# Kernel tuning notes

Measured on AMD Instinct MI355X. Metric: run time of the kernel, lower is better.

## Reference

```python
import jax, jax.numpy as jnp
import numpy as np

B, N, M = 2, 2048, 2048
Q_DIM = 1024
HEADS = 8
DIM_HEAD = 64
INNER = HEADS * DIM_HEAD  # 512


def setup_inputs() -> dict:
    key = jax.random.key(0)
    ks = jax.random.split(key, 7)
    s_in = 1.0 / np.sqrt(Q_DIM)
    s_out = 1.0 / np.sqrt(INNER)
    return {
        "x": jax.random.normal(ks[0], (B, N, Q_DIM), dtype=jnp.float32),
        "context": jax.random.normal(ks[1], (B, M, Q_DIM), dtype=jnp.float32),
        "Wq": jax.random.normal(ks[2], (Q_DIM, INNER), dtype=jnp.float32) * s_in,
        "Wk": jax.random.normal(ks[3], (Q_DIM, INNER), dtype=jnp.float32) * s_in,
        "Wv": jax.random.normal(ks[4], (Q_DIM, INNER), dtype=jnp.float32) * s_in,
        "Wo": jax.random.normal(ks[5], (INNER, Q_DIM), dtype=jnp.float32) * s_out,
        "bo": jax.random.normal(ks[6], (Q_DIM,), dtype=jnp.float32) * 0.01,
    }


def reference(x, context, Wq, Wk, Wv, Wo, bo):
    scale = DIM_HEAD ** (-0.5)
    # projections, split heads: [b, n, inner] -> [b, h, n, d]
    def split_heads(t):
        b, n, _ = t.shape
        return t.reshape(b, n, HEADS, DIM_HEAD).transpose(0, 2, 1, 3)
    q = split_heads(x @ Wq)
    k = split_heads(context @ Wk)
    v = split_heads(context @ Wv)
    sim = jnp.einsum('bhid,bhjd->bhij', q, k) * scale  # [b,h,n,m] full score matrix
    attn = jax.nn.softmax(sim, axis=-1)
    out = jnp.einsum('bhij,bhjd->bhid', attn, v)       # [b,h,n,d]
    out = out.transpose(0, 2, 1, 3).reshape(x.shape[0], x.shape[1], INNER)
    return out @ Wo + bo
```

## Files before the change

kernel.cpp:

```cpp
#include <hip/hip_runtime.h>

typedef __attribute__((ext_vector_type(8))) short short8;
typedef __attribute__((ext_vector_type(4))) short bf16x4;
typedef __attribute__((ext_vector_type(4))) float floatx4;
typedef __attribute__((ext_vector_type(4))) float f32x4;

__device__ __forceinline__ short f2bf(float f) {
    union { float f; unsigned u; } v;
    v.f = f;
    unsigned r = v.u + 0x7fffu + ((v.u >> 16) & 1u);
    return (short)(r >> 16);
}
__device__ __forceinline__ short8 cvt8(f32x4 a, f32x4 b) {
    short8 r;
    r[0] = f2bf(a[0]); r[1] = f2bf(a[1]); r[2] = f2bf(a[2]); r[3] = f2bf(a[3]);
    r[4] = f2bf(b[0]); r[5] = f2bf(b[1]); r[6] = f2bf(b[2]); r[7] = f2bf(b[3]);
    return r;
}
__device__ __forceinline__ bf16x4 pack4(float a, float b, float c, float d) {
    union { float f; unsigned u; } x;
    unsigned ua, ub, uc, ud;
    x.f = a; ua = (x.u + 0x8000u) >> 16;
    x.f = b; ub = (x.u + 0x8000u) >> 16;
    x.f = c; uc = (x.u + 0x8000u) >> 16;
    x.f = d; ud = (x.u + 0x8000u) >> 16;
    union { bf16x4 s; unsigned u2[2]; } r;
    r.u2[0] = ua | (ub << 16);
    r.u2[1] = uc | (ud << 16);
    return r.s;
}

#define MFMA_BF16(a, b, c) __builtin_amdgcn_mfma_f32_16x16x32_bf16((a), (b), (c), 0, 0, 0)

__device__ __forceinline__ floatx4 mfma16(bf16x4 a, bf16x4 b, floatx4 c) {
#if __has_builtin(__builtin_amdgcn_mfma_f32_16x16x16bf16_1k)
    return __builtin_amdgcn_mfma_f32_16x16x16bf16_1k(a, b, c, 0, 0, 0);
#else
    floatx4 d;
    asm volatile("v_mfma_f32_16x16x16_bf16 %0, %1, %2, %3"
                 : "=&v"(d) : "v"(a), "v"(b), "v"(c));
    return d;
#endif
}

__device__ __forceinline__ float fast_exp2(float x) {
#if __has_builtin(__builtin_amdgcn_exp2f)
    return __builtin_amdgcn_exp2f(x);
#else
    return exp2f(x);
#endif
}

#define QSCALE_LOG2E 0.18033688011112042f

__global__ __launch_bounds__(256) void wfrag_all(const float* __restrict__ Wq,
                                                 const float* __restrict__ Wk,
                                                 const float* __restrict__ Wv,
                                                 const float* __restrict__ Wo,
                                                 short* __restrict__ WqF,
                                                 short* __restrict__ WkF,
                                                 short* __restrict__ WvF,
                                                 short* __restrict__ WoF) {
    const int z = blockIdx.y;
    const float* src = (z == 0) ? Wq : (z == 1) ? Wk : (z == 2) ? Wv : Wo;
    short* dst = (z == 0) ? WqF : (z == 1) ? WkF : (z == 2) ? WvF : WoF;
    const int nbits = (z < 3) ? 9 : 10;
    const int N = 1 << nbits;
    const int t = blockIdx.x * 256 + threadIdx.x;
    const int kb = t >> nbits;
    const int n = t & (N - 1);
    const float* s = src + (size_t)(kb * 8) * N + n;
    short8 v;
#pragma unroll
    for (int j = 0; j < 8; ++j) v[j] = f2bf(s[(size_t)j * N]);
    *(short8*)(dst + (size_t)t * 8) = v;
}

__global__ __launch_bounds__(256, 3) void gemm_qkv(const float* __restrict__ x,
                                                   const float* __restrict__ ctx,
                                                   const short* __restrict__ WqF,
                                                   const short* __restrict__ WkF,
                                                   const short* __restrict__ WvF,
                                                   short* __restrict__ Qw,
                                                   short* __restrict__ Kw,
                                                   short* __restrict__ Vtw) {
    const int z = blockIdx.z;
    const float* A  = (z == 0) ? x : ctx;
    const short* WF = (z == 0) ? WqF : (z == 1) ? WkF : WvF;
    const int tid = threadIdx.x;
    const int w = tid >> 6;
    const int lane = tid & 63;
    const int quad = lane >> 4, ln = lane & 15;
    const int wr = w >> 1, wc = w & 1;
    const int row0 = blockIdx.x * 64;
    const int col0 = blockIdx.y * 128;

    __shared__ __align__(16) short Alds[2][2048];

    const int srow = tid >> 2;
    const int sseg = tid & 3;
    const float* aG = A + (size_t)(row0 + srow) * 1024 + sseg * 8;

    const short* bG[4];
#pragma unroll
    for (int t = 0; t < 4; ++t)
        bG[t] = WF + ((size_t)quad * 512 + col0 + wc * 64 + t * 16 + ln) * 8;

    floatx4 acc[2][4] = {};
    f32x4 aR[2][2];
    short8 bR[2][4];

    auto loadA = [&](int it, int set) {
        aR[set][0] = *(const f32x4*)(aG + it * 32);
        aR[set][1] = *(const f32x4*)(aG + it * 32 + 4);
    };
    auto writeA = [&](int buf, int set) {
        *(short8*)(&Alds[buf][(sseg * 64 + srow) * 8]) = cvt8(aR[set][0], aR[set][1]);
    };
    auto loadB = [&](int it, int set) {
#pragma unroll
        for (int t = 0; t < 4; ++t)
            bR[set][t] = *(const short8*)(bG[t] + (size_t)it * 16384);
    };

    loadA(0, 0);
    writeA(0, 0);
    loadA(1, 1);
    loadB(0, 0);
    __syncthreads();

    const int nsteps = 1024 / 32;
    for (int it = 0; it < nsteps; ++it) {
        const int buf = it & 1;
        if (it + 2 < nsteps) loadA(it + 2, it & 1);
        if (it + 1 < nsteps) {
            loadB(it + 1, (it + 1) & 1);
            writeA(buf ^ 1, (it + 1) & 1);
        }
        short8 af[2];
#pragma unroll
        for (int i = 0; i < 2; ++i)
            af[i] = *(const short8*)(&Alds[buf][quad * 512 + (wr * 32 + i * 16 + ln) * 8]);
#pragma unroll
        for (int i = 0; i < 2; ++i)
#pragma unroll
            for (int t = 0; t < 4; ++t)
                acc[i][t] = MFMA_BF16(af[i], bR[it & 1][t], acc[i][t]);
        __syncthreads();
    }

    const float oscale = (z == 0) ? QSCALE_LOG2E : 1.0f;
    short* dst = (z == 0) ? Qw : (z == 1) ? Kw : Vtw;
#pragma unroll
    for (int i = 0; i < 2; ++i)
#pragma unroll
        for (int t = 0; t < 4; ++t)
#pragma unroll
            for (int r = 0; r < 4; ++r) {
                const int R = row0 + wr * 32 + i * 16 + quad * 4 + r;
                const int C = col0 + wc * 64 + t * 16 + ln;
                const int b = R >> 11, n = R & 2047;
                const int h = C >> 6, d = C & 63;
                const short val = f2bf(acc[i][t][r] * oscale);
                if (z < 2)
                    dst[((b * 8 + h) * 2048 + n) * 64 + d] = val;
                else
                    dst[((b * 8 + h) * 64 + d) * 2048 + n] = val;
            }
}

__global__ __launch_bounds__(256, 2) void attn_kernel(const short* __restrict__ Q,
                                                      const short* __restrict__ K,
                                                      const short* __restrict__ Vt,
                                                      short* __restrict__ Aw) {
    const int tid = threadIdx.x;
    const int w = tid >> 6;
    const int lane = tid & 63;
    const int quad = lane >> 4;
    const int ln = lane & 15;
    const int q0 = blockIdx.x * 64;
    const int bh = blockIdx.y;

    __shared__ __align__(16) short klds[2][64][72];
    __shared__ __align__(16) short vlds[2][64][72];

    const short* Qbh = Q + bh * 2048 * 64;
    const short* Kbh = K + bh * 2048 * 64;
    const short* Vbh = Vt + bh * 64 * 2048;

    short8 qf[2];
    {
        const int qrow = q0 + w * 16 + ln;
        qf[0] = *(const short8*)(Qbh + qrow * 64 + quad * 8);
        qf[1] = *(const short8*)(Qbh + qrow * 64 + 32 + quad * 8);
    }

    floatx4 ot[4] = {};
    float lp = 0.f;

    const int sr = tid >> 3;
    const int sc = (tid & 7) * 8;

    auto computeTile = [&](int b) {
        short8 kf[8];
#pragma unroll
        for (int t = 0; t < 4; ++t)
#pragma unroll
            for (int ks = 0; ks < 2; ++ks)
                kf[t * 2 + ks] = *(const short8*)(&klds[b][t * 16 + ln][ks * 32 + quad * 8]);
        bf16x4 vf[16];
#pragma unroll
        for (int dt = 0; dt < 4; ++dt)
#pragma unroll
            for (int t = 0; t < 4; ++t)
                vf[dt * 4 + t] = *(const bf16x4*)(&vlds[b][dt * 16 + ln][t * 16 + quad * 4]);

        floatx4 s[4] = {};
#pragma unroll
        for (int ks = 0; ks < 2; ++ks)
#pragma unroll
            for (int t = 0; t < 4; ++t)
                s[t] = MFMA_BF16(kf[t * 2 + ks], qf[ks], s[t]);

        bf16x4 pf[4];
#pragma unroll
        for (int t = 0; t < 4; ++t) {
            float p0 = fast_exp2(s[t][0]);
            float p1 = fast_exp2(s[t][1]);
            float p2 = fast_exp2(s[t][2]);
            float p3 = fast_exp2(s[t][3]);
            lp += (p0 + p1) + (p2 + p3);
            pf[t] = pack4(p0, p1, p2, p3);
        }
#pragma unroll
        for (int t = 0; t < 4; ++t)
#pragma unroll
            for (int dt = 0; dt < 4; ++dt)
                ot[dt] = mfma16(vf[dt * 4 + t], pf[t], ot[dt]);
    };

    const int nt = 2048 / 64;

    {
        short8 k0 = *(const short8*)(Kbh + tid * 8);
        short8 k1 = *(const short8*)(Kbh + (tid + 256) * 8);
        short8 v0 = *(const short8*)(Vbh + sr * 2048 + sc);
        short8 v1 = *(const short8*)(Vbh + (sr + 32) * 2048 + sc);
        *(short8*)(&klds[0][sr][sc]) = k0;
        *(short8*)(&klds[0][sr + 32][sc]) = k1;
        *(short8*)(&vlds[0][sr][sc]) = v0;
        *(short8*)(&vlds[0][sr + 32][sc]) = v1;
    }
    __syncthreads();

    for (int it = 0; it < nt; ++it) {
        short8 k0, k1, v0, v1;
        const bool more = (it + 1 < nt);
        if (more) {
            const int jn = (it + 1) * 64;
            k0 = *(const short8*)(Kbh + jn * 64 + tid * 8);
            k1 = *(const short8*)(Kbh + jn * 64 + (tid + 256) * 8);
            v0 = *(const short8*)(Vbh + sr * 2048 + jn + sc);
            v1 = *(const short8*)(Vbh + (sr + 32) * 2048 + jn + sc);
        }
        computeTile(it & 1);
        if (more) {
            const int nb = (it + 1) & 1;
            *(short8*)(&klds[nb][sr][sc]) = k0;
            *(short8*)(&klds[nb][sr + 32][sc]) = k1;
            *(short8*)(&vlds[nb][sr][sc]) = v0;
            *(short8*)(&vlds[nb][sr + 32][sc]) = v1;
        }
        __syncthreads();
    }

    lp += __shfl_xor(lp, 16);
    lp += __shfl_xor(lp, 32);
    const float invL = 1.0f / lp;

    const int n = q0 + w * 16 + ln;
    const int b = bh >> 3, h = bh & 7;
    short* abase = Aw + ((size_t)(b * 2048 + n) * 512) + h * 64 + quad * 4;
#pragma unroll
    for (int dt = 0; dt < 4; ++dt)
        *(bf16x4*)(abase + dt * 16) =
            pack4(ot[dt][0] * invL, ot[dt][1] * invL, ot[dt][2] * invL, ot[dt][3] * invL);
}

__global__ __launch_bounds__(256, 2) void gemm_final(const short* __restrict__ A,
                                                     const short* __restrict__ WoF,
                                                     const float* __restrict__ bias,
                                                     float* __restrict__ out) {
    const int tid = threadIdx.x;
    const int w = tid >> 6;
    const int lane = tid & 63;
    const int quad = lane >> 4, ln = lane & 15;
    const int wr = w >> 1, wc = w & 1;
    const int row0 = blockIdx.x * 64;
    const int col0 = blockIdx.y * 128;

    __shared__ __align__(16) short Alds[2][2048];

    const int srow = tid >> 2;
    const int sseg = tid & 3;
    const short* aG = A + (size_t)(row0 + srow) * 512 + sseg * 8;

    const short* bG[4];
#pragma unroll
    for (int t = 0; t < 4; ++t)
        bG[t] = WoF + ((size_t)quad * 1024 + col0 + wc * 64 + t * 16 + ln) * 8;

    floatx4 acc[2][4] = {};
    short8 aR[2];
    short8 bR[2][4];

    auto loadA = [&](int it, int set) { aR[set] = *(const short8*)(aG + it * 32); };
    auto writeA = [&](int buf, int set) {
        *(short8*)(&Alds[buf][(sseg * 64 + srow) * 8]) = aR[set];
    };
    auto loadB = [&](int it, int set) {
#pragma unroll
        for (int t = 0; t < 4; ++t)
            bR[set][t] = *(const short8*)(bG[t] + (size_t)it * 32768);
    };

    loadA(0, 0);
    writeA(0, 0);
    loadA(1, 1);
    loadB(0, 0);
    __syncthreads();

    const int nsteps = 512 / 32;
    for (int it = 0; it < nsteps; ++it) {
        const int buf = it & 1;
        if (it + 2 < nsteps) loadA(it + 2, it & 1);
        if (it + 1 < nsteps) {
            loadB(it + 1, (it + 1) & 1);
            writeA(buf ^ 1, (it + 1) & 1);
        }
        short8 af[2];
#pragma unroll
        for (int i = 0; i < 2; ++i)
            af[i] = *(const short8*)(&Alds[buf][quad * 512 + (wr * 32 + i * 16 + ln) * 8]);
#pragma unroll
        for (int i = 0; i < 2; ++i)
#pragma unroll
            for (int t = 0; t < 4; ++t)
                acc[i][t] = MFMA_BF16(af[i], bR[it & 1][t], acc[i][t]);
        __syncthreads();
    }

#pragma unroll
    for (int i = 0; i < 2; ++i)
#pragma unroll
        for (int t = 0; t < 4; ++t)
#pragma unroll
            for (int r = 0; r < 4; ++r) {
                const int R = row0 + wr * 32 + i * 16 + quad * 4 + r;
                const int C = col0 + wc * 64 + t * 16 + ln;
                out[(size_t)R * 1024 + C] = acc[i][t][r] + bias[C];
            }
}

extern "C" void kernel_launch(void* const* d_in, const int* in_sizes, int n_in,
                              void* d_out, int out_size, void* d_ws, size_t ws_size,
                              hipStream_t stream) {
    const float* x   = (const float*)d_in[0];
    const float* ctx = (const float*)d_in[1];
    const float* Wq  = (const float*)d_in[2];
    const float* Wk  = (const float*)d_in[3];
    const float* Wv  = (const float*)d_in[4];
    const float* Wo  = (const float*)d_in[5];
    const float* bo  = (const float*)d_in[6];
    float* out = (float*)d_out;

    char* ws = (char*)d_ws;
    size_t off = 0;
    auto alloc = [&](size_t bytes) { char* p = ws + off; off += (bytes + 255) & ~(size_t)255; return p; };

    short* WqF  = (short*)alloc(512 * 1024 * 2);
    short* WkF  = (short*)alloc(512 * 1024 * 2);
    short* WvF  = (short*)alloc(512 * 1024 * 2);
    short* WoF  = (short*)alloc(1024 * 512 * 2);
    short* Qw   = (short*)alloc((size_t)16 * 2048 * 64 * 2);
    short* Kw   = (short*)alloc((size_t)16 * 2048 * 64 * 2);
    short* Vtw  = (short*)alloc((size_t)16 * 2048 * 64 * 2);
    short* Aw   = (short*)alloc((size_t)4096 * 512 * 2);

    wfrag_all<<<dim3(256, 4), 256, 0, stream>>>(Wq, Wk, Wv, Wo, WqF, WkF, WvF, WoF);

    gemm_qkv<<<dim3(64, 4, 3), 256, 0, stream>>>(x, ctx, WqF, WkF, WvF, Qw, Kw, Vtw);

    attn_kernel<<<dim3(32, 16), 256, 0, stream>>>(Qw, Kw, Vtw, Aw);

    gemm_final<<<dim3(64, 8), 256, 0, stream>>>(Aw, WoF, bo, out);
}
```

Baseline: 167.9 us.

## Pre-convert activations to fragment-major bf16 layout and drop LDS staging in GEMMs

```diff
diff --git a/kernel.cpp b/kernel.cpp
--- a/kernel.cpp
+++ b/kernel.cpp
@@ -76,8 +76,42 @@
     *(short8*)(dst + (size_t)t * 8) = v;
 }
 
-__global__ __launch_bounds__(256, 3) void gemm_qkv(const float* __restrict__ x,
-                                                   const float* __restrict__ ctx,
+__global__ __launch_bounds__(256) void afrag(const float* __restrict__ x,
+                                             const float* __restrict__ ctx,
+                                             short* __restrict__ AxF,
+                                             short* __restrict__ AcF) {
+    const float* src = (blockIdx.z == 0) ? x : ctx;
+    short* dst = (blockIdx.z == 0) ? AxF : AcF;
+    const int r0 = blockIdx.x * 64;
+    const int k0 = blockIdx.y * 64;
+    __shared__ short tile[64][72];
+    const int tid = threadIdx.x;
+    {
+        const int seg = tid & 15;
+        const int rbase = tid >> 4;
+#pragma unroll
+        for (int i = 0; i < 4; ++i) {
+            const int row = rbase + i * 16;
+            f32x4 v = *(const f32x4*)(src + (size_t)(r0 + row) * 1024 + k0 + seg * 4);
+#pragma unroll
+            for (int jj = 0; jj < 4; ++jj) tile[row][seg * 4 + jj] = f2bf(v[jj]);
+        }
+    }
+    __syncthreads();
+    {
+        const int kbl = tid >> 5;
+        const int rbase = tid & 31;
+#pragma unroll
+        for (int j = 0; j < 2; ++j) {
+            const int row = rbase + j * 32;
+            short8 v = *(const short8*)(&tile[row][kbl * 8]);
+            *(short8*)(dst + ((size_t)(k0 / 8 + kbl) * 4096 + r0 + row) * 8) = v;
+        }
+    }
+}
+
+__global__ __launch_bounds__(256, 4) void gemm_qkv(const short* __restrict__ AxF,
+                                                   const short* __restrict__ AcF,
                                                    const short* __restrict__ WqF,
                                                    const short* __restrict__ WkF,
                                                    const short* __restrict__ WvF,
@@ -85,7 +119,7 @@
                                                    short* __restrict__ Kw,
                                                    short* __restrict__ Vtw) {
     const int z = blockIdx.z;
-    const float* A  = (z == 0) ? x : ctx;
+    const short* AF = (z == 0) ? AxF : AcF;
     const short* WF = (z == 0) ? WqF : (z == 1) ? WkF : WvF;
     const int tid = threadIdx.x;
     const int w = tid >> 6;
@@ -95,58 +129,33 @@
     const int row0 = blockIdx.x * 64;
     const int col0 = blockIdx.y * 128;
 
-    __shared__ __align__(16) short Alds[2][2048];
-
-    const int srow = tid >> 2;
-    const int sseg = tid & 3;
-    const float* aG = A + (size_t)(row0 + srow) * 1024 + sseg * 8;
-
-    const short* bG[4];
-#pragma unroll
-    for (int t = 0; t < 4; ++t)
-        bG[t] = WF + ((size_t)quad * 512 + col0 + wc * 64 + t * 16 + ln) * 8;
+    const short* aBase = AF + ((size_t)quad * 4096 + row0 + wr * 32 + ln) * 8;
+    const short* bBase = WF + ((size_t)quad * 512 + col0 + wc * 64 + ln) * 8;
 
     floatx4 acc[2][4] = {};
-    f32x4 aR[2][2];
-    short8 bR[2][4];
-
-    auto loadA = [&](int it, int set) {
-        aR[set][0] = *(const f32x4*)(aG + it * 32);
-        aR[set][1] = *(const f32x4*)(aG + it * 32 + 4);
+    short8 aR[3][2], bR[3][4];
+
+    auto loadStep = [&](int it) {
+        const int s = it % 3;
+#pragma unroll
+        for (int i = 0; i < 2; ++i)
+            aR[s][i] = *(const short8*)(aBase + (size_t)it * 131072 + i * 128);
+#pragma unroll
+        for (int t = 0; t < 4; ++t)
+            bR[s][t] = *(const short8*)(bBase + (size_t)it * 16384 + t * 128);
     };
-    auto writeA = [&](int buf, int set) {
-        *(short8*)(&Alds[buf][(sseg * 64 + srow) * 8]) = cvt8(aR[set][0], aR[set][1]);
-    };
-    auto loadB = [&](int it, int set) {
-#pragma unroll
-        for (int t = 0; t < 4; ++t)
-            bR[set][t] = *(const short8*)(bG[t] + (size_t)it * 16384);
-    };
-
-    loadA(0, 0);
-    writeA(0, 0);
-    loadA(1, 1);
-    loadB(0, 0);
-    __syncthreads();
-
-    const int nsteps = 1024 / 32;
-    for (int it = 0; it < nsteps; ++it) {
-        const int buf = it & 1;
-        if (it + 2 < nsteps) loadA(it + 2, it & 1);
-        if (it + 1 < nsteps) {
-            loadB(it + 1, (it + 1) & 1);
-            writeA(buf ^ 1, (it + 1) & 1);
-        }
-        short8 af[2];
+
+    loadStep(0);
+    loadStep(1);
+#pragma unroll
+    for (int it = 0; it < 32; ++it) {
+        if (it + 2 < 32) loadStep(it + 2);
+        const int s = it % 3;
 #pragma unroll
         for (int i = 0; i < 2; ++i)
-            af[i] = *(const short8*)(&Alds[buf][quad * 512 + (wr * 32 + i * 16 + ln) * 8]);
-#pragma unroll
-        for (int i = 0; i < 2; ++i)
 #pragma unroll
             for (int t = 0; t < 4; ++t)
-                acc[i][t] = MFMA_BF16(af[i], bR[it & 1][t], acc[i][t]);
-        __syncthreads();
+                acc[i][t] = MFMA_BF16(aR[s][i], bR[s][t], acc[i][t]);
     }
 
     const float oscale = (z == 0) ? QSCALE_LOG2E : 1.0f;
@@ -172,7 +181,7 @@
 __global__ __launch_bounds__(256, 2) void attn_kernel(const short* __restrict__ Q,
                                                       const short* __restrict__ K,
                                                       const short* __restrict__ Vt,
-                                                      short* __restrict__ Aw) {
+                                                      short* __restrict__ AwF) {
     const int tid = threadIdx.x;
     const int w = tid >> 6;
     const int lane = tid & 63;
@@ -280,14 +289,17 @@
 
     const int n = q0 + w * 16 + ln;
     const int b = bh >> 3, h = bh & 7;
-    short* abase = Aw + ((size_t)(b * 2048 + n) * 512) + h * 64 + quad * 4;
-#pragma unroll
-    for (int dt = 0; dt < 4; ++dt)
-        *(bf16x4*)(abase + dt * 16) =
-            pack4(ot[dt][0] * invL, ot[dt][1] * invL, ot[dt][2] * invL, ot[dt][3] * invL);
-}
-
-__global__ __launch_bounds__(256, 2) void gemm_final(const short* __restrict__ A,
+    const int R = b * 2048 + n;
+#pragma unroll
+    for (int dt = 0; dt < 4; ++dt) {
+        const int kb = h * 8 + dt * 2 + (quad >> 1);
+        short* p = AwF + ((size_t)kb * 4096 + R) * 8 + (quad & 1) * 4;
+        *(bf16x4*)p = pack4(ot[dt][0] * invL, ot[dt][1] * invL,
+                            ot[dt][2] * invL, ot[dt][3] * invL);
+    }
+}
+
+__global__ __launch_bounds__(256, 4) void gemm_final(const short* __restrict__ AwF,
                                                      const short* __restrict__ WoF,
                                                      const float* __restrict__ bias,
                                                      float* __restrict__ out) {
@@ -299,55 +311,33 @@
     const int row0 = blockIdx.x * 64;
     const int col0 = blockIdx.y * 128;
 
-    __shared__ __align__(16) short Alds[2][2048];
-
-    const int srow = tid >> 2;
-    const int sseg = tid & 3;
-    const short* aG = A + (size_t)(row0 + srow) * 512 + sseg * 8;
-
-    const short* bG[4];
-#pragma unroll
-    for (int t = 0; t < 4; ++t)
-        bG[t] = WoF + ((size_t)quad * 1024 + col0 + wc * 64 + t * 16 + ln) * 8;
+    const short* aBase = AwF + ((size_t)quad * 4096 + row0 + wr * 32 + ln) * 8;
+    const short* bBase = WoF + ((size_t)quad * 1024 + col0 + wc * 64 + ln) * 8;
 
     floatx4 acc[2][4] = {};
-    short8 aR[2];
-    short8 bR[2][4];
-
-    auto loadA = [&](int it, int set) { aR[set] = *(const short8*)(aG + it * 32); };
-    auto writeA = [&](int buf, int set) {
-        *(short8*)(&Alds[buf][(sseg * 64 + srow) * 8]) = aR[set];
+    short8 aR[3][2], bR[3][4];
+
+    auto loadStep = [&](int it) {
+        const int s = it % 3;
+#pragma unroll
+        for (int i = 0; i < 2; ++i)
+            aR[s][i] = *(const short8*)(aBase + (size_t)it * 131072 + i * 128);
+#pragma unroll
+        for (int t = 0; t < 4; ++t)
+            bR[s][t] = *(const short8*)(bBase + (size_t)it * 32768 + t * 128);
     };
-    auto loadB = [&](int it, int set) {
-#pragma unroll
-        for (int t = 0; t < 4; ++t)
-            bR[set][t] = *(const short8*)(bG[t] + (size_t)it * 32768);
-    };
-
-    loadA(0, 0);
-    writeA(0, 0);
-    loadA(1, 1);
-    loadB(0, 0);
-    __syncthreads();
-
-    const int nsteps = 512 / 32;
-    for (int it = 0; it < nsteps; ++it) {
-        const int buf = it & 1;
-        if (it + 2 < nsteps) loadA(it + 2, it & 1);
-        if (it + 1 < nsteps) {
-            loadB(it + 1, (it + 1) & 1);
-            writeA(buf ^ 1, (it + 1) & 1);
-        }
-        short8 af[2];
+
+    loadStep(0);
+    loadStep(1);
+#pragma unroll
+    for (int it = 0; it < 16; ++it) {
+        if (it + 2 < 16) loadStep(it + 2);
+        const int s = it % 3;
 #pragma unroll
         for (int i = 0; i < 2; ++i)
-            af[i] = *(const short8*)(&Alds[buf][quad * 512 + (wr * 32 + i * 16 + ln) * 8]);
-#pragma unroll
-        for (int i = 0; i < 2; ++i)
 #pragma unroll
             for (int t = 0; t < 4; ++t)
-                acc[i][t] = MFMA_BF16(af[i], bR[it & 1][t], acc[i][t]);
-        __syncthreads();
+                acc[i][t] = MFMA_BF16(aR[s][i], bR[s][t], acc[i][t]);
     }
 
 #pragma unroll
@@ -382,16 +372,19 @@
     short* WkF  = (short*)alloc(512 * 1024 * 2);
     short* WvF  = (short*)alloc(512 * 1024 * 2);
     short* WoF  = (short*)alloc(1024 * 512 * 2);
+    short* AxF  = (short*)alloc((size_t)4096 * 1024 * 2);
+    short* AcF  = (short*)alloc((size_t)4096 * 1024 * 2);
     short* Qw   = (short*)alloc((size_t)16 * 2048 * 64 * 2);
     short* Kw   = (short*)alloc((size_t)16 * 2048 * 64 * 2);
     short* Vtw  = (short*)alloc((size_t)16 * 2048 * 64 * 2);
-    short* Aw   = (short*)alloc((size_t)4096 * 512 * 2);
+    short* AwF  = (short*)alloc((size_t)4096 * 512 * 2);
 
     wfrag_all<<<dim3(256, 4), 256, 0, stream>>>(Wq, Wk, Wv, Wo, WqF, WkF, WvF, WoF);
-
-    gemm_qkv<<<dim3(64, 4, 3), 256, 0, stream>>>(x, ctx, WqF, WkF, WvF, Qw, Kw, Vtw);
-
-    attn_kernel<<<dim3(32, 16), 256, 0, stream>>>(Qw, Kw, Vtw, Aw);
-
-    gemm_final<<<dim3(64, 8), 256, 0, stream>>>(Aw, WoF, bo, out);
-}
+    afrag<<<dim3(64, 16, 2), 256, 0, stream>>>(x, ctx, AxF, AcF);
+
+    gemm_qkv<<<dim3(64, 4, 3), 256, 0, stream>>>(AxF, AcF, WqF, WkF, WvF, Qw, Kw, Vtw);
+
+    attn_kernel<<<dim3(32, 16), 256, 0, stream>>>(Qw, Kw, Vtw, AwF);
+
+    gemm_final<<<dim3(64, 8), 256, 0, stream>>>(AwF, WoF, bo, out);
+}
```

New measurement: 166.4 us. About the same (-0.9%).
